# Performance work log

Measured on AMD Instinct MI355X. Metric: run time of the kernel, lower is better.

Reference implementation:

```python
import jax, jax.numpy as jnp
import numpy as np

B, S, D_IN, D_OUT = 4, 2048, 1024, 1024
USE_MASK = True


def setup_inputs() -> dict:
    key = jax.random.key(0)
    ks = jax.random.split(key, 6)
    return {
        "inputs_for_keys": jax.random.normal(ks[0], (B, S, D_IN), jnp.float32),
        "inputs_for_values": jax.random.normal(ks[1], (B, S, D_IN), jnp.float32),
        "inputs_for_queries": jax.random.normal(ks[2], (B, S, D_IN), jnp.float32),
        "WK": jax.random.normal(ks[3], (D_IN, D_OUT), jnp.float32) * 0.1,
        "WV": jax.random.normal(ks[4], (D_IN, D_OUT), jnp.float32) * 0.1,
        "WQ": jax.random.normal(ks[5], (D_IN, D_OUT), jnp.float32) * 0.1,
    }


def reference(inputs_for_keys, inputs_for_values, inputs_for_queries, WK, WV, WQ):
    # projections: [B,S,Din] @ [Din,Dout] -> [B,S,Dout]
    K = jnp.einsum("bsd,de->bse", inputs_for_keys, WK)
    V = jnp.einsum("bsd,de->bse", inputs_for_values, WV)
    Q = jnp.einsum("bsd,de->bse", inputs_for_queries, WQ)

    dk = jnp.asarray(K.shape[2], jnp.float32)
    # scores: [B, Sq, Sk]
    score = jnp.einsum("bqd,bkd->bqk", Q, K) / jnp.sqrt(dk)
    if USE_MASK:
        # causal: -inf strictly above diagonal (j > i), matching the
        # transposed tril(-1) * -inf construction in the original.
        q_idx = jnp.arange(S)[:, None]
        k_idx = jnp.arange(S)[None, :]
        mask = jnp.where(k_idx > q_idx, -jnp.inf, 0.0).astype(score.dtype)
        score = score + mask[None, :, :]
    soft_score = jax.nn.softmax(score, axis=-1)
    return jnp.einsum("bqk,bkd->bqd", soft_score, V)
```

## Files before the change

kernel.cpp:

```cpp
#include <hip/hip_runtime.h>
#include <hip/hip_bf16.h>

typedef unsigned short u16;
typedef _Float16 f16;
typedef __attribute__((ext_vector_type(8))) short s16x8;
typedef __attribute__((ext_vector_type(8))) _Float16 f16x8;
typedef __attribute__((ext_vector_type(4))) float f32x4;
typedef __attribute__((ext_vector_type(4))) unsigned short u16x4;

template <typename T>
__device__ __forceinline__ auto mfma_try(T a, T b, f32x4 c, int)
    -> decltype(__builtin_amdgcn_mfma_f32_16x16x32_f16(a, b, c, 0, 0, 0)) {
  return __builtin_amdgcn_mfma_f32_16x16x32_f16(a, b, c, 0, 0, 0);
}
template <typename T>
__device__ __forceinline__ f32x4 mfma_try(T a, T b, f32x4 c, long) {
  return __builtin_amdgcn_mfma_f32_16x16x32_f16(
      __builtin_bit_cast(f16x8, a), __builtin_bit_cast(f16x8, b), c, 0, 0, 0);
}
__device__ __forceinline__ f32x4 MFMA16(s16x8 a, s16x8 b, f32x4 c) {
  return mfma_try(a, b, c, 0);
}

__device__ __forceinline__ void gload16(const void* g, void* s) {
  __builtin_amdgcn_global_load_lds(
      (const __attribute__((address_space(1))) void*)g,
      (__attribute__((address_space(3))) void*)s, 16, 0, 0);
}

__device__ __forceinline__ u16 f2h(float x) {
  f16 h = (f16)x;
  u16 u;
  __builtin_memcpy(&u, &h, 2);
  return u;
}
__device__ __forceinline__ float h2f(u16 u) {
  f16 h;
  __builtin_memcpy(&h, &u, 2);
  return (float)h;
}

#define LDS_SWZ(r, cb) ((cb) ^ (((r)&7) << 4))

struct Geom {
  int srow[4], scol[4];
  int w, l, wr, wc;
};

__device__ __forceinline__ Geom make_geom() {
  Geom g;
  int tid = threadIdx.x;
  g.w = tid >> 6; g.l = tid & 63;
  g.wr = g.w >> 1; g.wc = g.w & 1;
#pragma unroll
  for (int i = 0; i < 4; ++i) {
    int off = i * 4096 + g.w * 1024 + g.l * 16;
    int r = off >> 7, cb = off & 127;
    g.srow[i] = r;
    g.scol[i] = LDS_SWZ(r, cb) >> 1;
  }
  return g;
}

__device__ __forceinline__ void stage(const u16* pan, int ld, int k0,
                                      char* lds, const Geom& g) {
#pragma unroll
  for (int i = 0; i < 4; ++i)
    gload16(pan + (long)g.srow[i] * ld + k0 + g.scol[i],
            lds + i * 4096 + g.w * 1024);
}

__device__ __forceinline__ void compute_step(const char* lA, const char* lB,
                                             const Geom& g, f32x4 acc[4][4]) {
#pragma unroll
  for (int ks = 0; ks < 2; ++ks) {
    s16x8 af[4], bg[4];
#pragma unroll
    for (int m = 0; m < 4; ++m) {
      int r = g.wr * 64 + m * 16 + (g.l & 15);
      int cb = ks * 64 + ((g.l >> 4) << 4);
      af[m] = *(const s16x8*)(lA + r * 128 + LDS_SWZ(r, cb));
    }
#pragma unroll
    for (int n = 0; n < 4; ++n) {
      int r = g.wc * 64 + n * 16 + (g.l & 15);
      int cb = ks * 64 + ((g.l >> 4) << 4);
      bg[n] = *(const s16x8*)(lB + r * 128 + LDS_SWZ(r, cb));
    }
#pragma unroll
    for (int m = 0; m < 4; ++m)
#pragma unroll
      for (int n = 0; n < 4; ++n)
        acc[m][n] = MFMA16(af[m], bg[n], acc[m][n]);
  }
}

__device__ __forceinline__ void gemm_core_sb(const u16* Apan, int lda,
                                             const u16* Bpan, int ldb,
                                             int nsteps, char* lA, char* lB,
                                             const Geom& g, f32x4 acc[4][4]) {
  for (int t = 0; t < nsteps; ++t) {
    stage(Apan, lda, t * 64, lA, g);
    stage(Bpan, ldb, t * 64, lB, g);
    __syncthreads();
    compute_step(lA, lB, g, acc);
    __syncthreads();
  }
}

__device__ __forceinline__ void gemm_core_db(const u16* Apan, int lda,
                                             const u16* Bpan, int ldb,
                                             int nsteps, char* lA, char* lB,
                                             const Geom& g, f32x4 acc[4][4]) {
  stage(Apan, lda, 0, lA, g);
  stage(Bpan, ldb, 0, lB, g);
  __syncthreads();
  for (int t = 0; t < nsteps; ++t) {
    int cur = (t & 1) << 14;
    if (t + 1 < nsteps) {
      int nxt = ((t + 1) & 1) << 14;
      stage(Apan, lda, (t + 1) * 64, lA + nxt, g);
      stage(Bpan, ldb, (t + 1) * 64, lB + nxt, g);
    }
    compute_step(lA + cur, lB + cur, g, acc);
    if (t + 1 < nsteps) __syncthreads();
  }
}

__global__ __launch_bounds__(256, 3) void proj_kernel(
    const u16* __restrict__ xk, const u16* __restrict__ xq, const u16* __restrict__ xv,
    const u16* __restrict__ wk, const u16* __restrict__ wq, const u16* __restrict__ wv,
    u16* __restrict__ K, u16* __restrict__ Q, u16* __restrict__ Vt) {
  __shared__ char lds[32768];
  const int y = blockIdx.y;
  const u16* X = y == 0 ? xk : (y == 1 ? xq : xv);
  const u16* W = y == 0 ? wk : (y == 1 ? wq : wv);
  const int bx = blockIdx.x;
  const int swz = (bx & 7) * 64 + (bx >> 3);
  const int tm = swz >> 3, tn = swz & 7;
  Geom g = make_geom();
  f32x4 acc[4][4] = {};
  gemm_core_sb(X + (long)tm * 128 * 1024, 1024, W + (long)tn * 128 * 1024,
               1024, 16, lds, lds + 16384, g, acc);
  const int rg0 = tm * 128 + g.wr * 64, cg0 = tn * 128 + g.wc * 64;
  if (y < 2) {
    u16* C = y == 0 ? K : Q;
#pragma unroll
    for (int m = 0; m < 4; ++m)
#pragma unroll
      for (int n = 0; n < 4; ++n)
#pragma unroll
        for (int j = 0; j < 4; ++j) {
          int rg = rg0 + m * 16 + ((g.l >> 4) << 2) + j;
          int cg = cg0 + n * 16 + (g.l & 15);
          C[(long)rg * 1024 + cg] = f2h(acc[m][n][j]);
        }
  } else {
#pragma unroll
    for (int m = 0; m < 4; ++m) {
      int rg = rg0 + m * 16 + ((g.l >> 4) << 2);
      int b = rg >> 11, rl = rg & 2047;
#pragma unroll
      for (int n = 0; n < 4; ++n) {
        int cg = cg0 + n * 16 + (g.l & 15);
        u16x4 pk;
#pragma unroll
        for (int j = 0; j < 4; ++j) pk[j] = f2h(acc[m][n][j]);
        *(u16x4*)(Vt + (long)b * (1024 * 2048) + (long)cg * 2048 + rl) = pk;
      }
    }
  }
}

__global__ __launch_bounds__(256, 2) void qkt_kernel(
    const u16* __restrict__ Q, const u16* __restrict__ K, u16* __restrict__ S) {
  __shared__ char lds[65536];
  const int bx = blockIdx.x;
  const int swz = (bx & 7) * 68 + (bx >> 3);
  const int b = swz / 136;
  int t = swz - b * 136;
  int tm = 0;
  while (t > tm) { t -= tm + 1; ++tm; }
  const int tn = t;
  Geom g = make_geom();
  f32x4 acc[4][4] = {};
  const u16* Qb = Q + (long)b * 2048 * 1024;
  const u16* Kb = K + (long)b * 2048 * 1024;
  gemm_core_db(Qb + (long)tm * 128 * 1024, 1024, Kb + (long)tn * 128 * 1024,
               1024, 16, lds, lds + 32768, g, acc);
  u16* Sb = S + (long)b * 2048 * 2048;
  const int rg0 = tm * 128 + g.wr * 64, cg0 = tn * 128 + g.wc * 64;
#pragma unroll
  for (int m = 0; m < 4; ++m)
#pragma unroll
    for (int n = 0; n < 4; ++n)
#pragma unroll
      for (int j = 0; j < 4; ++j) {
        int rg = rg0 + m * 16 + ((g.l >> 4) << 2) + j;
        int cg = cg0 + n * 16 + (g.l & 15);
        Sb[(long)rg * 2048 + cg] = f2h(acc[m][n][j]);
      }
}

__global__ __launch_bounds__(256, 2) void pv_kernel(
    const u16* __restrict__ P, const u16* __restrict__ Vt, float* __restrict__ O) {
  __shared__ char lds[65536];
  const int bx = blockIdx.x;
  const int swz = (bx & 7) * 64 + (bx >> 3);
  const int b = swz >> 7, loc = swz & 127;
  const int tm = loc >> 3, tn = loc & 7;
  Geom g = make_geom();
  f32x4 acc[4][4] = {};
  gemm_core_db(P + ((long)b * 2048 + tm * 128) * 2048, 2048,
               Vt + (long)b * 1024 * 2048 + (long)tn * 128 * 2048, 2048,
               (tm + 1) * 2, lds, lds + 32768, g, acc);
  const int rg0 = tm * 128 + g.wr * 64, cg0 = tn * 128 + g.wc * 64;
#pragma unroll
  for (int m = 0; m < 4; ++m)
#pragma unroll
    for (int n = 0; n < 4; ++n)
#pragma unroll
      for (int j = 0; j < 4; ++j) {
        int rg = rg0 + m * 16 + ((g.l >> 4) << 2) + j;
        int cg = cg0 + n * 16 + (g.l & 15);
        O[((long)b * 2048 + rg) * 1024 + cg] = acc[m][n][j];
      }
}

__global__ __launch_bounds__(256) void softmax_causal(
    const u16* __restrict__ S, u16* __restrict__ P) {
  const int bid = blockIdx.x;
  const int b = bid >> 10, i0 = bid & 1023;
  const int tid = threadIdx.x;
  const int l = tid & 63, w = tid >> 6;
  const int base = tid * 8;
  __shared__ float red[8];

#pragma unroll
  for (int ph = 0; ph < 2; ++ph) {
    const int i_q = ph ? (2047 - i0) : i0;
    const long row = (long)b * 2048 + i_q;
    const int klim = ((i_q >> 7) + 1) << 7;
    const u16* sr = S + row * 2048;
    u16* pr = P + row * 2048;

    float v[8];
    float m = -INFINITY;
    if (base <= i_q) {
      s16x8 raw = *(const s16x8*)(sr + base);
#pragma unroll
      for (int j = 0; j < 8; ++j) {
        float x = h2f((u16)raw[j]);
        x = (base + j <= i_q) ? x : -INFINITY;
        v[j] = x;
        m = fmaxf(m, x);
      }
    } else {
#pragma unroll
      for (int j = 0; j < 8; ++j) v[j] = -INFINITY;
    }
    for (int o = 32; o; o >>= 1) m = fmaxf(m, __shfl_xor(m, o, 64));
    if (l == 0) red[w] = m;
    __syncthreads();
    m = fmaxf(fmaxf(red[0], red[1]), fmaxf(red[2], red[3]));

    float s = 0.f;
#pragma unroll
    for (int j = 0; j < 8; ++j) {
      v[j] = __expf(v[j] - m);
      s += v[j];
    }
    for (int o = 32; o; o >>= 1) s += __shfl_xor(s, o, 64);
    if (l == 0) red[4 + w] = s;
    __syncthreads();
    s = (red[4] + red[5]) + (red[6] + red[7]);
    float inv = 1.0f / s;

    if (base < klim) {
      s16x8 o;
#pragma unroll
      for (int j = 0; j < 8; ++j) o[j] = (short)f2h(v[j] * inv);
      *(s16x8*)(pr + base) = o;
    }
    __syncthreads();
  }
}

__global__ __launch_bounds__(256) void cast_all_kernel(
    const float* __restrict__ x0, const float* __restrict__ x1,
    const float* __restrict__ x2, u16* __restrict__ o0, u16* __restrict__ o1,
    u16* __restrict__ o2, const float* __restrict__ wk,
    const float* __restrict__ wv, const float* __restrict__ wq,
    u16* __restrict__ ok, u16* __restrict__ ov, u16* __restrict__ oq) {
  const int bid = blockIdx.x;
  if (bid < 12288) {
    const int y = bid >> 12;
    const float* in = y == 0 ? x0 : (y == 1 ? x1 : x2);
    u16* out = y == 0 ? o0 : (y == 1 ? o1 : o2);
    long i = ((long)(bid & 4095) * 256 + threadIdx.x) * 8;
    f32x4 a = *(const f32x4*)(in + i);
    f32x4 b = *(const f32x4*)(in + i + 4);
    s16x8 o;
#pragma unroll
    for (int j = 0; j < 4; ++j) {
      o[j] = (short)f2h(a[j]);
      o[4 + j] = (short)f2h(b[j]);
    }
    *(s16x8*)(out + i) = o;
  } else {
    __shared__ float tile[32][33];
    const int t = bid - 12288;
    const int z = t >> 10;
    const int loc = t & 1023;
    const int bx = loc & 31, by = loc >> 5;
    const float* w = z == 0 ? wk : (z == 1 ? wv : wq);
    u16* o = z == 0 ? ok : (z == 1 ? ov : oq);
    const float scale = (z == 2) ? 0.03125f : 1.0f;
    const int lx = threadIdx.x & 31, ly = threadIdx.x >> 5;
#pragma unroll
    for (int j = 0; j < 32; j += 8)
      tile[ly + j][lx] = w[(long)(by * 32 + ly + j) * 1024 + bx * 32 + lx];
    __syncthreads();
#pragma unroll
    for (int j = 0; j < 32; j += 8)
      o[(long)(bx * 32 + ly + j) * 1024 + by * 32 + lx] =
          f2h(tile[lx][ly + j] * scale);
  }
}

extern "C" void kernel_launch(void* const* d_in, const int* in_sizes, int n_in,
                              void* d_out, int out_size, void* d_ws, size_t ws_size,
                              hipStream_t stream) {
  const float* Xk = (const float*)d_in[0];
  const float* Xv = (const float*)d_in[1];
  const float* Xq = (const float*)d_in[2];
  const float* WK = (const float*)d_in[3];
  const float* WV = (const float*)d_in[4];
  const float* WQ = (const float*)d_in[5];

  const int Bn = 4, S = 2048, D = 1024;
  const long NX = (long)Bn * S * D;

  const size_t r0 = (size_t)Bn * S * S * 4;
  const size_t r1 = r0 + 3ull * D * D * 2;
  const size_t r2 = r1 + 2ull * NX * 2;
  const size_t NEED = r2 + (size_t)NX * 2;
  if (ws_size < NEED) {
    hipMemsetAsync(d_out, 0, (size_t)out_size * 4, stream);
    return;
  }
  char* ws = (char*)d_ws;
  u16* xkb = (u16*)ws;
  u16* xvb = xkb + NX;
  u16* xqb = xvb + NX;
  u16* scoresH = (u16*)ws;
  u16* wkt = (u16*)(ws + r0);
  u16* wvt = wkt + D * D;
  u16* wqt = wvt + D * D;
  u16* Kb = (u16*)(ws + r1);
  u16* Qb = Kb + NX;
  u16* Pb = (u16*)(ws + r1);
  u16* Vt = (u16*)(ws + r2);

  cast_all_kernel<<<dim3(15360), 256, 0, stream>>>(Xk, Xv, Xq, xkb, xvb, xqb,
                                                   WK, WV, WQ, wkt, wvt, wqt);
  proj_kernel<<<dim3(512, 3), 256, 0, stream>>>(xkb, xqb, xvb, wkt, wqt, wvt,
                                                Kb, Qb, Vt);
  qkt_kernel<<<dim3(544), 256, 0, stream>>>(Qb, Kb, scoresH);
  softmax_causal<<<dim3(4096), 256, 0, stream>>>(scoresH, Pb);
  pv_kernel<<<dim3(512), 256, 0, stream>>>(Pb, Vt, (float*)d_out);
}
```

Baseline: 157.2 us.

## Enlarge projection GEMM tile to 128x256 with per-wave 128x64 outputs

The projection kernel now computes a 128x256 output tile per block instead of 128x128, with each of the four waves owning a 128x64 slice (8x4 MFMA accumulators). It stages the A panel once and a wider B panel into 48KB of LDS, which halves the grid and raises arithmetic intensity per loaded byte. In exchange, register pressure doubles for accumulators, occupancy drops (launch bounds 3 to 2), and there are fewer blocks to fill the GPU.

```diff
diff --git a/kernel.cpp b/kernel.cpp
--- a/kernel.cpp
+++ b/kernel.cpp
@@ -92,19 +92,6 @@
 #pragma unroll
       for (int n = 0; n < 4; ++n)
         acc[m][n] = MFMA16(af[m], bg[n], acc[m][n]);
-  }
-}
-
-__device__ __forceinline__ void gemm_core_sb(const u16* Apan, int lda,
-                                             const u16* Bpan, int ldb,
-                                             int nsteps, char* lA, char* lB,
-                                             const Geom& g, f32x4 acc[4][4]) {
-  for (int t = 0; t < nsteps; ++t) {
-    stage(Apan, lda, t * 64, lA, g);
-    stage(Bpan, ldb, t * 64, lB, g);
-    __syncthreads();
-    compute_step(lA, lB, g, acc);
-    __syncthreads();
   }
 }
 
@@ -127,42 +114,90 @@
   }
 }
 
-__global__ __launch_bounds__(256, 3) void proj_kernel(
+__global__ __launch_bounds__(256, 2) void proj_kernel(
     const u16* __restrict__ xk, const u16* __restrict__ xq, const u16* __restrict__ xv,
     const u16* __restrict__ wk, const u16* __restrict__ wq, const u16* __restrict__ wv,
     u16* __restrict__ K, u16* __restrict__ Q, u16* __restrict__ Vt) {
-  __shared__ char lds[32768];
+  __shared__ char lds[49152];
+  char* lA = lds;
+  char* lB = lds + 16384;
   const int y = blockIdx.y;
   const u16* X = y == 0 ? xk : (y == 1 ? xq : xv);
   const u16* W = y == 0 ? wk : (y == 1 ? wq : wv);
   const int bx = blockIdx.x;
-  const int swz = (bx & 7) * 64 + (bx >> 3);
-  const int tm = swz >> 3, tn = swz & 7;
-  Geom g = make_geom();
-  f32x4 acc[4][4] = {};
-  gemm_core_sb(X + (long)tm * 128 * 1024, 1024, W + (long)tn * 128 * 1024,
-               1024, 16, lds, lds + 16384, g, acc);
-  const int rg0 = tm * 128 + g.wr * 64, cg0 = tn * 128 + g.wc * 64;
+  const int swz = (bx & 7) * 32 + (bx >> 3);
+  const int tm = swz >> 2, tn = swz & 3;
+  const int tid = threadIdx.x;
+  const int w = tid >> 6, l = tid & 63;
+
+  int srow[8], scol[8];
+#pragma unroll
+  for (int i = 0; i < 8; ++i) {
+    int off = i * 4096 + tid * 16;
+    int r = off >> 7, cb = off & 127;
+    srow[i] = r;
+    scol[i] = LDS_SWZ(r, cb) >> 1;
+  }
+  const u16* Apan = X + (long)tm * 128 * 1024;
+  const u16* Bpan = W + (long)tn * 256 * 1024;
+
+  f32x4 acc[8][4] = {};
+  for (int t = 0; t < 16; ++t) {
+    const int k0 = t * 64;
+#pragma unroll
+    for (int i = 0; i < 4; ++i)
+      gload16(Apan + (long)srow[i] * 1024 + k0 + scol[i],
+              lA + i * 4096 + w * 1024);
+#pragma unroll
+    for (int i = 0; i < 8; ++i)
+      gload16(Bpan + (long)srow[i] * 1024 + k0 + scol[i],
+              lB + i * 4096 + w * 1024);
+    __syncthreads();
+#pragma unroll
+    for (int ks = 0; ks < 2; ++ks) {
+      s16x8 af[8], bg[4];
+      const int cb = ks * 64 + ((l >> 4) << 4);
+#pragma unroll
+      for (int m = 0; m < 8; ++m) {
+        int r = m * 16 + (l & 15);
+        af[m] = *(const s16x8*)(lA + r * 128 + LDS_SWZ(r, cb));
+      }
+#pragma unroll
+      for (int n = 0; n < 4; ++n) {
+        int r = w * 64 + n * 16 + (l & 15);
+        bg[n] = *(const s16x8*)(lB + r * 128 + LDS_SWZ(r, cb));
+      }
+#pragma unroll
+      for (int m = 0; m < 8; ++m)
+#pragma unroll
+        for (int n = 0; n < 4; ++n)
+          acc[m][n] = MFMA16(af[m], bg[n], acc[m][n]);
+    }
+    __syncthreads();
+  }
+
+  const int rg0 = tm * 128;
+  const int cg0 = tn * 256 + w * 64;
   if (y < 2) {
     u16* C = y == 0 ? K : Q;
 #pragma unroll
-    for (int m = 0; m < 4; ++m)
+    for (int m = 0; m < 8; ++m)
 #pragma unroll
       for (int n = 0; n < 4; ++n)
 #pragma unroll
         for (int j = 0; j < 4; ++j) {
-          int rg = rg0 + m * 16 + ((g.l >> 4) << 2) + j;
-          int cg = cg0 + n * 16 + (g.l & 15);
+          int rg = rg0 + m * 16 + ((l >> 4) << 2) + j;
+          int cg = cg0 + n * 16 + (l & 15);
           C[(long)rg * 1024 + cg] = f2h(acc[m][n][j]);
         }
   } else {
 #pragma unroll
-    for (int m = 0; m < 4; ++m) {
-      int rg = rg0 + m * 16 + ((g.l >> 4) << 2);
+    for (int m = 0; m < 8; ++m) {
+      int rg = rg0 + m * 16 + ((l >> 4) << 2);
       int b = rg >> 11, rl = rg & 2047;
 #pragma unroll
       for (int n = 0; n < 4; ++n) {
-        int cg = cg0 + n * 16 + (g.l & 15);
+        int cg = cg0 + n * 16 + (l & 15);
         u16x4 pk;
 #pragma unroll
         for (int j = 0; j < 4; ++j) pk[j] = f2h(acc[m][n][j]);
@@ -364,7 +399,7 @@
 
   cast_all_kernel<<<dim3(15360), 256, 0, stream>>>(Xk, Xv, Xq, xkb, xvb, xqb,
                                                    WK, WV, WQ, wkt, wvt, wqt);
-  proj_kernel<<<dim3(512, 3), 256, 0, stream>>>(xkb, xqb, xvb, wkt, wqt, wvt,
+  proj_kernel<<<dim3(256, 3), 256, 0, stream>>>(xkb, xqb, xvb, wkt, wqt, wvt,
                                                 Kb, Qb, Vt);
   qkt_kernel<<<dim3(544), 256, 0, stream>>>(Qb, Kb, scoresH);
   softmax_causal<<<dim3(4096), 256, 0, stream>>>(scoresH, Pb);
```

New measurement: 161.7 us. 2.9% more time.
